# Kernel optimization log

Hardware: AMD Instinct MI355X
Metric: run time of the kernel (lower is better)

The kernel has to match this reference:

```python
import jax, jax.numpy as jnp
import numpy as np

N_NODES = 100000
N_EDGES = 1600000
D_IN = 128
D_OUT = 128


def setup_inputs() -> dict:
    key = jax.random.key(0)
    ks = jax.random.split(key, 8)
    x = jax.random.normal(ks[0], (N_NODES, D_IN), dtype=jnp.float32)
    edge_index = jax.random.randint(ks[1], (2, N_EDGES), 0, N_NODES, dtype=jnp.int64)
    s1 = 1.0 / np.sqrt(D_IN)
    s2 = 1.0 / np.sqrt(D_OUT)
    # SAGEConv: lin_l acts on aggregated neighbors (has bias), lin_r on self (no bias)
    Wl1 = jax.random.uniform(ks[2], (D_OUT, D_IN), jnp.float32, -s1, s1)
    Wr1 = jax.random.uniform(ks[3], (D_OUT, D_IN), jnp.float32, -s1, s1)
    b1 = jnp.zeros((D_OUT,), jnp.float32)
    Wl2 = jax.random.uniform(ks[4], (D_OUT, D_OUT), jnp.float32, -s2, s2)
    Wr2 = jax.random.uniform(ks[5], (D_OUT, D_OUT), jnp.float32, -s2, s2)
    b2 = jnp.zeros((D_OUT,), jnp.float32)
    return {"x": x, "edge_index": edge_index, "Wl1": Wl1, "Wr1": Wr1, "b1": b1,
            "Wl2": Wl2, "Wr2": Wr2, "b2": b2}


def _sage_conv(x, src, dst, Wl, Wr, b, n_nodes):
    # mean aggregation of source features at destination nodes
    agg = jax.ops.segment_sum(x[src], dst, num_segments=n_nodes)  # [N, d]
    deg = jax.ops.segment_sum(jnp.ones((src.shape[0],), x.dtype), dst, num_segments=n_nodes)
    mean = agg / jnp.maximum(deg, 1.0)[:, None]  # isolated nodes -> 0 (PyG scatter-mean)
    return mean @ Wl.T + b + x @ Wr.T


def reference(x, edge_index, Wl1, Wr1, b1, Wl2, Wr2, b2):
    src, dst = edge_index[0], edge_index[1]
    n = x.shape[0]
    h = _sage_conv(x, src, dst, Wl1, Wr1, b1, n)
    h = _sage_conv(h, src, dst, Wl2, Wr2, b2, n)
    return h
```

## Files before the change

kernel.cpp:

```cpp
#include <hip/hip_runtime.h>
#include <hip/hip_bf16.h>

#define D 128
#define SCAN_CHUNK 1024
#define TE 4096

typedef __attribute__((ext_vector_type(8))) short bf16x8;
typedef __attribute__((ext_vector_type(4))) float f32x4;
typedef __attribute__((ext_vector_type(2))) float f32x2;

__device__ __forceinline__ bool ei_is64(const int* ei32) {
    return (ei32[1] | ei32[3] | ei32[5] | ei32[7]) == 0;
}
__device__ __forceinline__ int get_idx(const void* ei, bool is64, long long pos) {
    return is64 ? (int)((const long long*)ei)[pos] : ((const int*)ei)[pos];
}

__global__ __launch_bounds__(256) void prep_kernel(
    const float* __restrict__ x, unsigned* __restrict__ xq, long long ND, int ncvt,
    const float* __restrict__ Wl1, const float* __restrict__ Wr1,
    const float* __restrict__ Wl2, const float* __restrict__ Wr2,
    ushort* __restrict__ Wf1, ushort* __restrict__ Wf2,
    const void* __restrict__ ei, int E, int NB, int NBLK, int SH,
    int* __restrict__ histT) {
    __shared__ int h[512];
    const int t = threadIdx.x;
    int bid = blockIdx.x;

    if (bid < ncvt) {
        long long i = ((long long)bid * 256 + t) * 8;
        if (i + 7 < ND) {
            float4 v0 = *reinterpret_cast<const float4*>(x + i);
            float4 v1 = *reinterpret_cast<const float4*>(x + i + 4);
            int p0 = __builtin_amdgcn_cvt_pk_fp8_f32(v0.x, v0.y, 0, false);
            p0 = __builtin_amdgcn_cvt_pk_fp8_f32(v0.z, v0.w, p0, true);
            int p1 = __builtin_amdgcn_cvt_pk_fp8_f32(v1.x, v1.y, 0, false);
            p1 = __builtin_amdgcn_cvt_pk_fp8_f32(v1.z, v1.w, p1, true);
            *reinterpret_cast<uint2*>(reinterpret_cast<unsigned char*>(xq) + i) =
                make_uint2((unsigned)p0, (unsigned)p1);
        } else {
            for (; i < ND; ++i) {
                int pk = __builtin_amdgcn_cvt_pk_fp8_f32(x[i], x[i], 0, false);
                reinterpret_cast<unsigned char*>(xq)[i] = (unsigned char)(pk & 0xff);
            }
        }
        return;
    }
    bid -= ncvt;
    if (bid < 32) {
        int gid = bid * 256 + t;
        int id = gid & 4095;
        const float* Wl = Wl1; const float* Wr = Wr1; ushort* Wf = Wf1;
        if (gid >= 4096) { Wl = Wl2; Wr = Wr2; Wf = Wf2; }
        int lane = id & 63, s = (id >> 6) & 7, j = id >> 9;
        int c = j * 16 + (lane & 15);
        int k = s * 32 + ((lane >> 4) << 3);
        const float* src = (k < 128) ? (Wl + c * 128 + k) : (Wr + c * 128 + (k - 128));
        float4 v0 = *reinterpret_cast<const float4*>(src);
        float4 v1 = *reinterpret_cast<const float4*>(src + 4);
        __hip_bfloat16 o[8];
        o[0] = __float2bfloat16(v0.x); o[1] = __float2bfloat16(v0.y);
        o[2] = __float2bfloat16(v0.z); o[3] = __float2bfloat16(v0.w);
        o[4] = __float2bfloat16(v1.x); o[5] = __float2bfloat16(v1.y);
        o[6] = __float2bfloat16(v1.z); o[7] = __float2bfloat16(v1.w);
        *reinterpret_cast<uint4*>(Wf + (size_t)id * 8) = *reinterpret_cast<uint4*>(o);
        return;
    }
    bid -= 32;
    for (int b = t; b < 512; b += 256) h[b] = 0;
    bool is64 = ei_is64((const int*)ei);
    __syncthreads();
    const int base = bid * TE;
    for (int i = t; i < TE; i += 256) {
        int e = base + i;
        if (e < E) {
            int d = get_idx(ei, is64, (long long)E + e);
            atomicAdd(&h[d >> SH], 1);
        }
    }
    __syncthreads();
    for (int b = t; b < NB; b += 256) histT[b * NBLK + bid] = h[b];
}

__global__ __launch_bounds__(256) void scan_partial_kernel(int* __restrict__ arr, int Ntot,
                                                           int* __restrict__ bsum) {
    __shared__ int ws[256];
    const int t = threadIdx.x;
    const int i0 = blockIdx.x * SCAN_CHUNK + t * 4;
    int4 v = {0, 0, 0, 0};
    if (i0 + 3 < Ntot) {
        v = *reinterpret_cast<const int4*>(arr + i0);
    } else {
        if (i0 < Ntot) v.x = arr[i0];
        if (i0 + 1 < Ntot) v.y = arr[i0 + 1];
        if (i0 + 2 < Ntot) v.z = arr[i0 + 2];
        if (i0 + 3 < Ntot) v.w = arr[i0 + 3];
    }
    ws[t] = v.x + v.y + v.z + v.w;
    __syncthreads();
    for (int off = 1; off < 256; off <<= 1) {
        int val = (t >= off) ? ws[t - off] : 0;
        __syncthreads();
        ws[t] += val;
        __syncthreads();
    }
    int ex = t ? ws[t - 1] : 0;
    int e0 = ex, e1 = ex + v.x, e2 = e1 + v.y, e3 = e2 + v.z;
    if (i0 + 3 < Ntot) {
        *reinterpret_cast<int4*>(arr + i0) = make_int4(e0, e1, e2, e3);
    } else {
        if (i0 < Ntot) arr[i0] = e0;
        if (i0 + 1 < Ntot) arr[i0 + 1] = e1;
        if (i0 + 2 < Ntot) arr[i0 + 2] = e2;
        if (i0 + 3 < Ntot) arr[i0 + 3] = e3;
    }
    if (t == 255) bsum[blockIdx.x] = ws[255];
}

__device__ __forceinline__ void scan_bsum_lds(const int* __restrict__ bsum, int nb2,
                                              int* sb) {
    const int t = threadIdx.x;
    sb[t] = (t < nb2) ? bsum[t] : 0;
    __syncthreads();
    for (int off = 1; off < 256; off <<= 1) {
        int v = (t >= off) ? sb[t - off] : 0;
        __syncthreads();
        sb[t] += v;
        __syncthreads();
    }
}

__global__ __launch_bounds__(256) void part_scatter_kernel(const void* __restrict__ ei, int E,
                                                           int NB, int NBLK, int SH,
                                                           const int* __restrict__ histT,
                                                           const int* __restrict__ bsum,
                                                           int nb2,
                                                           unsigned* __restrict__ ebuf) {
    __shared__ int cur[512];
    __shared__ int sb[256];
    const int t = threadIdx.x;
    bool is64 = ei_is64((const int*)ei);
    scan_bsum_lds(bsum, nb2, sb);
    for (int b = t; b < NB; b += 256) {
        int idx = b * NBLK + blockIdx.x;
        int c = idx >> 10;
        cur[b] = histT[idx] + (c ? sb[c - 1] : 0);
    }
    __syncthreads();
    const int base = blockIdx.x * TE;
    for (int i = t; i < TE; i += 256) {
        int e = base + i;
        if (e < E) {
            int s = get_idx(ei, is64, e);
            int d = get_idx(ei, is64, (long long)E + e);
            int pos = atomicAdd(&cur[d >> SH], 1);
            ebuf[pos] = (unsigned)s | ((unsigned)(d & ((1 << SH) - 1)) << 24);
        }
    }
}

__global__ __launch_bounds__(256) void bucket_csr_kernel(const unsigned* __restrict__ ebuf,
                                                         const int* __restrict__ histT,
                                                         const int* __restrict__ bsum,
                                                         int nb2,
                                                         int NB, int NBLK, int SH, int E,
                                                         int N, int* __restrict__ rs,
                                                         int* __restrict__ col) {
    const int b = blockIdx.x, t = threadIdx.x;
    const int nodes = 1 << SH;
    __shared__ int h[256];
    __shared__ int cur[256];
    __shared__ int sb[256];
    __shared__ int sse[2];
    scan_bsum_lds(bsum, nb2, sb);
    if (t == 0) {
        int i0 = b * NBLK;
        int c0 = i0 >> 10;
        sse[0] = histT[i0] + (c0 ? sb[c0 - 1] : 0);
        if (b + 1 < NB) {
            int i1 = (b + 1) * NBLK;
            int c1 = i1 >> 10;
            sse[1] = histT[i1] + (c1 ? sb[c1 - 1] : 0);
        } else {
            sse[1] = E;
        }
    }
    h[t] = 0;
    __syncthreads();
    const int bstart = sse[0], bend = sse[1];
    for (int i = bstart + t; i < bend; i += 256) {
        atomicAdd(&h[ebuf[i] >> 24], 1);
    }
    __syncthreads();
    for (int off = 1; off < nodes; off <<= 1) {
        int v = (t >= off) ? h[t - off] : 0;
        __syncthreads();
        h[t] += v;
        __syncthreads();
    }
    const int node0 = b << SH;
    {
        int node = node0 + t;
        if (node < N) rs[node] = bstart + h[t];
        cur[t] = bstart + (t ? h[t - 1] : 0);
    }
    __syncthreads();
    for (int i = bstart + t; i < bend; i += 256) {
        unsigned ed = ebuf[i];
        int pos = atomicAdd(&cur[ed >> 24], 1);
        col[pos] = (int)(ed & 0xFFFFFFu);
    }
}

__device__ __forceinline__ void acc8(f32x2& a0, f32x2& a1, f32x2& a2, f32x2& a3,
                                     uint2 d) {
    a0 += __builtin_amdgcn_cvt_pk_f32_fp8((int)d.x, false);
    a1 += __builtin_amdgcn_cvt_pk_f32_fp8((int)d.x, true);
    a2 += __builtin_amdgcn_cvt_pk_f32_fp8((int)d.y, false);
    a3 += __builtin_amdgcn_cvt_pk_f32_fp8((int)d.y, true);
}

__global__ __launch_bounds__(512) void aggregate_mean_fp8_kernel(
    const unsigned char* __restrict__ xq, const int* __restrict__ rs,
    const int* __restrict__ col, ushort* __restrict__ outm, int N) {
    __shared__ int s_start[32], s_end[32], s_map[32];
    const int t = threadIdx.x;
    if (t < 32) {
        int v = blockIdx.x * 32 + t;
        int st = 0, en = 0;
        if (v < N) { st = v ? rs[v - 1] : 0; en = rs[v]; }
        s_start[t] = st; s_end[t] = en;
    }
    __syncthreads();
    if (t < 32) {
        int d = s_end[t] - s_start[t];
        int r = 0;
#pragma unroll
        for (int j = 0; j < 32; ++j) {
            int dj = s_end[j] - s_start[j];
            r += (dj < d) || (dj == d && j < t);
        }
        s_map[r] = t;
    }
    __syncthreads();

    const int Q = t >> 4;
    const int li = s_map[Q];
    const int v = blockIdx.x * 32 + li;
    const int start = s_start[li], end = s_end[li];
    const unsigned lcoff = (unsigned)(t & 15) * 8u;

    f32x2 a0 = {0.f, 0.f}, a1 = {0.f, 0.f}, a2 = {0.f, 0.f}, a3 = {0.f, 0.f};
    int e = start;
    for (; e + 7 < end; e += 8) {
        int c0 = col[e], c1 = col[e + 1], c2 = col[e + 2], c3 = col[e + 3];
        int c4 = col[e + 4], c5 = col[e + 5], c6 = col[e + 6], c7 = col[e + 7];
        uint2 d0 = *reinterpret_cast<const uint2*>(xq + (((unsigned)c0) << 7) + lcoff);
        uint2 d1 = *reinterpret_cast<const uint2*>(xq + (((unsigned)c1) << 7) + lcoff);
        uint2 d2 = *reinterpret_cast<const uint2*>(xq + (((unsigned)c2) << 7) + lcoff);
        uint2 d3 = *reinterpret_cast<const uint2*>(xq + (((unsigned)c3) << 7) + lcoff);
        uint2 d4 = *reinterpret_cast<const uint2*>(xq + (((unsigned)c4) << 7) + lcoff);
        uint2 d5 = *reinterpret_cast<const uint2*>(xq + (((unsigned)c5) << 7) + lcoff);
        uint2 d6 = *reinterpret_cast<const uint2*>(xq + (((unsigned)c6) << 7) + lcoff);
        uint2 d7 = *reinterpret_cast<const uint2*>(xq + (((unsigned)c7) << 7) + lcoff);
        acc8(a0, a1, a2, a3, d0); acc8(a0, a1, a2, a3, d1);
        acc8(a0, a1, a2, a3, d2); acc8(a0, a1, a2, a3, d3);
        acc8(a0, a1, a2, a3, d4); acc8(a0, a1, a2, a3, d5);
        acc8(a0, a1, a2, a3, d6); acc8(a0, a1, a2, a3, d7);
    }
    if (e < end) {
        const int l = end - 1;
        int i1 = e + 1 < end ? e + 1 : l;
        int i2 = e + 2 < end ? e + 2 : l;
        int i3 = e + 3 < end ? e + 3 : l;
        int i4 = e + 4 < end ? e + 4 : l;
        int i5 = e + 5 < end ? e + 5 : l;
        int i6 = e + 6 < end ? e + 6 : l;
        int c0 = col[e], c1 = col[i1], c2 = col[i2], c3 = col[i3];
        int c4 = col[i4], c5 = col[i5], c6 = col[i6];
        uint2 d0 = *reinterpret_cast<const uint2*>(xq + (((unsigned)c0) << 7) + lcoff);
        uint2 d1 = *reinterpret_cast<const uint2*>(xq + (((unsigned)c1) << 7) + lcoff);
        uint2 d2 = *reinterpret_cast<const uint2*>(xq + (((unsigned)c2) << 7) + lcoff);
        uint2 d3 = *reinterpret_cast<const uint2*>(xq + (((unsigned)c3) << 7) + lcoff);
        uint2 d4 = *reinterpret_cast<const uint2*>(xq + (((unsigned)c4) << 7) + lcoff);
        uint2 d5 = *reinterpret_cast<const uint2*>(xq + (((unsigned)c5) << 7) + lcoff);
        uint2 d6 = *reinterpret_cast<const uint2*>(xq + (((unsigned)c6) << 7) + lcoff);
        d1.x = (e + 1 < end) ? d1.x : 0u; d1.y = (e + 1 < end) ? d1.y : 0u;
        d2.x = (e + 2 < end) ? d2.x : 0u; d2.y = (e + 2 < end) ? d2.y : 0u;
        d3.x = (e + 3 < end) ? d3.x : 0u; d3.y = (e + 3 < end) ? d3.y : 0u;
        d4.x = (e + 4 < end) ? d4.x : 0u; d4.y = (e + 4 < end) ? d4.y : 0u;
        d5.x = (e + 5 < end) ? d5.x : 0u; d5.y = (e + 5 < end) ? d5.y : 0u;
        d6.x = (e + 6 < end) ? d6.x : 0u; d6.y = (e + 6 < end) ? d6.y : 0u;
        acc8(a0, a1, a2, a3, d0); acc8(a0, a1, a2, a3, d1);
        acc8(a0, a1, a2, a3, d2); acc8(a0, a1, a2, a3, d3);
        acc8(a0, a1, a2, a3, d4); acc8(a0, a1, a2, a3, d5);
        acc8(a0, a1, a2, a3, d6);
    }
    if (v < N) {
        float inv = (end > start) ? 1.0f / (float)(end - start) : 0.f;
        __hip_bfloat16 o[8];
        o[0] = __float2bfloat16(a0.x * inv); o[1] = __float2bfloat16(a0.y * inv);
        o[2] = __float2bfloat16(a1.x * inv); o[3] = __float2bfloat16(a1.y * inv);
        o[4] = __float2bfloat16(a2.x * inv); o[5] = __float2bfloat16(a2.y * inv);
        o[6] = __float2bfloat16(a3.x * inv); o[7] = __float2bfloat16(a3.y * inv);
        *reinterpret_cast<uint4*>(outm + (size_t)v * D + ((t & 15) << 3)) =
            *reinterpret_cast<uint4*>(o);
    }
}

template <typename OutT, bool DUAL, bool SELFF32>
__global__ __launch_bounds__(512) void sage_mfma_kernel(
    const ushort* __restrict__ Ab, const void* __restrict__ Sb,
    const ushort* __restrict__ Wf, const float* __restrict__ bias,
    OutT* __restrict__ out, unsigned char* __restrict__ fq, int N) {
    __shared__ uint4 ldsB[4096];
    const int t = threadIdx.x;
    {
        const uint4* g = reinterpret_cast<const uint4*>(Wf);
#pragma unroll
        for (int i = 0; i < 8; ++i) ldsB[t + i * 512] = g[t + i * 512];
    }
    __syncthreads();

    const int lane = t & 63, w = t >> 6;
    const int lm = lane & 15;
    const int ksub = (lane >> 4) * 8;
    const int mbase = blockIdx.x * 128 + w * 16;

    int r0 = mbase + lm;
    if (r0 >= N) r0 = N - 1;

    f32x4 acc[8];
#pragma unroll
    for (int j = 0; j < 8; ++j) {
        float bv = bias[j * 16 + lm];
        acc[j] = {bv, bv, bv, bv};
    }

    const ushort* A0 = Ab + (size_t)r0 * D + ksub;
    const ushort* lB = reinterpret_cast<const ushort*>(ldsB) + lane * 8;

#pragma unroll
    for (int s = 0; s < 8; ++s) {
        bf16x8 a;
        if (s < 4) {
            a = *reinterpret_cast<const bf16x8*>(A0 + s * 32);
        } else if constexpr (SELFF32) {
            const float* S0 = (const float*)Sb + (size_t)r0 * D + (s - 4) * 32 + ksub;
            float4 v0 = *reinterpret_cast<const float4*>(S0);
            float4 v1 = *reinterpret_cast<const float4*>(S0 + 4);
            __hip_bfloat16 o[8];
            o[0] = __float2bfloat16(v0.x); o[1] = __float2bfloat16(v0.y);
            o[2] = __float2bfloat16(v0.z); o[3] = __float2bfloat16(v0.w);
            o[4] = __float2bfloat16(v1.x); o[5] = __float2bfloat16(v1.y);
            o[6] = __float2bfloat16(v1.z); o[7] = __float2bfloat16(v1.w);
            a = *reinterpret_cast<bf16x8*>(o);
        } else {
            const ushort* S0 = (const ushort*)Sb + (size_t)r0 * D + ksub;
            a = *reinterpret_cast<const bf16x8*>(S0 + (s - 4) * 32);
        }
#pragma unroll
        for (int j = 0; j < 8; ++j) {
            bf16x8 b = *reinterpret_cast<const bf16x8*>(lB + (j * 8 + s) * 512);
            acc[j] = __builtin_amdgcn_mfma_f32_16x16x32_bf16(a, b, acc[j], 0, 0, 0);
        }
    }

    const int rr = (lane >> 4) * 4;
#pragma unroll
    for (int r = 0; r < 4; ++r) {
        int row = mbase + rr + r;
        if (row < N) {
#pragma unroll
            for (int j = 0; j < 8; ++j) {
                float val = acc[j][r];
                if constexpr (sizeof(OutT) == 2)
                    out[(size_t)row * D + j * 16 + lm] = __float2bfloat16(val);
                else
                    out[(size_t)row * D + j * 16 + lm] = val;
                if constexpr (DUAL) {
                    int pk = __builtin_amdgcn_cvt_pk_fp8_f32(val, val, 0, false);
                    fq[(size_t)row * D + j * 16 + lm] = (unsigned char)(pk & 0xff);
                }
            }
        }
    }
}

extern "C" void kernel_launch(void* const* d_in, const int* in_sizes, int n_in,
                              void* d_out, int out_size, void* d_ws, size_t ws_size,
                              hipStream_t stream) {
    const float* x   = (const float*)d_in[0];
    const void*  ei  = d_in[1];
    const float* Wl1 = (const float*)d_in[2];
    const float* Wr1 = (const float*)d_in[3];
    const float* b1  = (const float*)d_in[4];
    const float* Wl2 = (const float*)d_in[5];
    const float* Wr2 = (const float*)d_in[6];
    const float* b2  = (const float*)d_in[7];
    float* out = (float*)d_out;

    const int N = in_sizes[0] / D;
    const int E = in_sizes[1] / 2;
    const long long ND = (long long)N * D;

    int SH = 8;
    while (((N + (1 << SH) - 1) >> SH) > 512) ++SH;
    const int NB = (N + (1 << SH) - 1) >> SH;
    const int NBLK = (E + TE - 1) / TE;
    const int Ntot = NB * NBLK;
    const int nb2 = (Ntot + SCAN_CHUNK - 1) / SCAN_CHUNK;

    ushort* meanb = (ushort*)d_ws;
    ushort* h1b   = meanb + ND;
    ushort* Wf1   = h1b + ND;
    ushort* Wf2   = Wf1 + 32768;
    int*    rs    = (int*)(Wf2 + 32768);
    int*    col   = rs + N;
    int*      histT = (int*)meanb;
    int*      bsum  = histT + Ntot;
    unsigned* ebuf  = (unsigned*)h1b;
    unsigned char* xq  = (unsigned char*)d_out;
    unsigned char* h1q = (unsigned char*)d_out + ND;

    const int ncvt = (int)((ND / 8 + 255) / 256);

    prep_kernel<<<ncvt + 32 + NBLK, 256, 0, stream>>>(
        x, (unsigned*)xq, ND, ncvt, Wl1, Wr1, Wl2, Wr2,
        Wf1, Wf2, ei, E, NB, NBLK, SH, histT);

    scan_partial_kernel<<<nb2, 256, 0, stream>>>(histT, Ntot, bsum);
    part_scatter_kernel<<<NBLK, 256, 0, stream>>>(ei, E, NB, NBLK, SH, histT, bsum, nb2, ebuf);
    bucket_csr_kernel<<<NB, 256, 0, stream>>>(ebuf, histT, bsum, nb2, NB, NBLK, SH, E, N, rs, col);

    const int agg_grid = (N + 31) / 32;
    const int gemm_grid = (N + 127) / 128;

    aggregate_mean_fp8_kernel<<<agg_grid, 512, 0, stream>>>(xq, rs, col, meanb, N);
    sage_mfma_kernel<__hip_bfloat16, true, true><<<gemm_grid, 512, 0, stream>>>(
        meanb, x, Wf1, b1, (__hip_bfloat16*)h1b, h1q, N);

    aggregate_mean_fp8_kernel<<<agg_grid, 512, 0, stream>>>(h1q, rs, col, meanb, N);
    sage_mfma_kernel<float, false, false><<<gemm_grid, 512, 0, stream>>>(
        meanb, h1b, Wf2, b2, out, nullptr, N);
}
```

Measured before the change: 164.0 us.

## Process two nodes per 16-lane group in aggregation, drop degree-sort scheduling

The mean-aggregation kernel now has each 16-thread group handle two destination nodes (v and v+16) with interleaved 8-edge gather batches, using 256-thread blocks instead of 512. The shared-memory degree ranking and its two __syncthreads are removed. The aim is more independent loads in flight per thread and less per-block setup. In exchange, per-thread register use goes up, and the two nodes in a group can have unbalanced degrees, which leaves lanes idle.

```diff
diff --git a/kernel.cpp b/kernel.cpp
--- a/kernel.cpp
+++ b/kernel.cpp
@@ -220,92 +220,107 @@
     a3 += __builtin_amdgcn_cvt_pk_f32_fp8((int)d.y, true);
 }
 
-__global__ __launch_bounds__(512) void aggregate_mean_fp8_kernel(
+__device__ __forceinline__ void gather_batch8(
+    const unsigned char* __restrict__ xq, const int* __restrict__ col, int e,
+    unsigned lcoff, f32x2& a0, f32x2& a1, f32x2& a2, f32x2& a3) {
+    int c0 = col[e], c1 = col[e + 1], c2 = col[e + 2], c3 = col[e + 3];
+    int c4 = col[e + 4], c5 = col[e + 5], c6 = col[e + 6], c7 = col[e + 7];
+    uint2 d0 = *reinterpret_cast<const uint2*>(xq + (((unsigned)c0) << 7) + lcoff);
+    uint2 d1 = *reinterpret_cast<const uint2*>(xq + (((unsigned)c1) << 7) + lcoff);
+    uint2 d2 = *reinterpret_cast<const uint2*>(xq + (((unsigned)c2) << 7) + lcoff);
+    uint2 d3 = *reinterpret_cast<const uint2*>(xq + (((unsigned)c3) << 7) + lcoff);
+    uint2 d4 = *reinterpret_cast<const uint2*>(xq + (((unsigned)c4) << 7) + lcoff);
+    uint2 d5 = *reinterpret_cast<const uint2*>(xq + (((unsigned)c5) << 7) + lcoff);
+    uint2 d6 = *reinterpret_cast<const uint2*>(xq + (((unsigned)c6) << 7) + lcoff);
+    uint2 d7 = *reinterpret_cast<const uint2*>(xq + (((unsigned)c7) << 7) + lcoff);
+    acc8(a0, a1, a2, a3, d0); acc8(a0, a1, a2, a3, d1);
+    acc8(a0, a1, a2, a3, d2); acc8(a0, a1, a2, a3, d3);
+    acc8(a0, a1, a2, a3, d4); acc8(a0, a1, a2, a3, d5);
+    acc8(a0, a1, a2, a3, d6); acc8(a0, a1, a2, a3, d7);
+}
+
+__device__ __forceinline__ void gather_masked(
+    const unsigned char* __restrict__ xq, const int* __restrict__ col, int e, int end,
+    unsigned lcoff, f32x2& a0, f32x2& a1, f32x2& a2, f32x2& a3) {
+    const int l = end - 1;
+    int i1 = e + 1 < end ? e + 1 : l;
+    int i2 = e + 2 < end ? e + 2 : l;
+    int i3 = e + 3 < end ? e + 3 : l;
+    int i4 = e + 4 < end ? e + 4 : l;
+    int i5 = e + 5 < end ? e + 5 : l;
+    int i6 = e + 6 < end ? e + 6 : l;
+    int c0 = col[e], c1 = col[i1], c2 = col[i2], c3 = col[i3];
+    int c4 = col[i4], c5 = col[i5], c6 = col[i6];
+    uint2 d0 = *reinterpret_cast<const uint2*>(xq + (((unsigned)c0) << 7) + lcoff);
+    uint2 d1 = *reinterpret_cast<const uint2*>(xq + (((unsigned)c1) << 7) + lcoff);
+    uint2 d2 = *reinterpret_cast<const uint2*>(xq + (((unsigned)c2) << 7) + lcoff);
+    uint2 d3 = *reinterpret_cast<const uint2*>(xq + (((unsigned)c3) << 7) + lcoff);
+    uint2 d4 = *reinterpret_cast<const uint2*>(xq + (((unsigned)c4) << 7) + lcoff);
+    uint2 d5 = *reinterpret_cast<const uint2*>(xq + (((unsigned)c5) << 7) + lcoff);
+    uint2 d6 = *reinterpret_cast<const uint2*>(xq + (((unsigned)c6) << 7) + lcoff);
+    d1.x = (e + 1 < end) ? d1.x : 0u; d1.y = (e + 1 < end) ? d1.y : 0u;
+    d2.x = (e + 2 < end) ? d2.x : 0u; d2.y = (e + 2 < end) ? d2.y : 0u;
+    d3.x = (e + 3 < end) ? d3.x : 0u; d3.y = (e + 3 < end) ? d3.y : 0u;
+    d4.x = (e + 4 < end) ? d4.x : 0u; d4.y = (e + 4 < end) ? d4.y : 0u;
+    d5.x = (e + 5 < end) ? d5.x : 0u; d5.y = (e + 5 < end) ? d5.y : 0u;
+    d6.x = (e + 6 < end) ? d6.x : 0u; d6.y = (e + 6 < end) ? d6.y : 0u;
+    acc8(a0, a1, a2, a3, d0); acc8(a0, a1, a2, a3, d1);
+    acc8(a0, a1, a2, a3, d2); acc8(a0, a1, a2, a3, d3);
+    acc8(a0, a1, a2, a3, d4); acc8(a0, a1, a2, a3, d5);
+    acc8(a0, a1, a2, a3, d6);
+}
+
+__device__ __forceinline__ void store_mean(ushort* __restrict__ outm, int v, int lc,
+                                           int deg, f32x2 a0, f32x2 a1, f32x2 a2,
+                                           f32x2 a3) {
+    float inv = (deg > 0) ? 1.0f / (float)deg : 0.f;
+    __hip_bfloat16 o[8];
+    o[0] = __float2bfloat16(a0.x * inv); o[1] = __float2bfloat16(a0.y * inv);
+    o[2] = __float2bfloat16(a1.x * inv); o[3] = __float2bfloat16(a1.y * inv);
+    o[4] = __float2bfloat16(a2.x * inv); o[5] = __float2bfloat16(a2.y * inv);
+    o[6] = __float2bfloat16(a3.x * inv); o[7] = __float2bfloat16(a3.y * inv);
+    *reinterpret_cast<uint4*>(outm + (size_t)v * D + (lc << 3)) =
+        *reinterpret_cast<uint4*>(o);
+}
+
+__global__ __launch_bounds__(256) void aggregate_mean_fp8_kernel(
     const unsigned char* __restrict__ xq, const int* __restrict__ rs,
     const int* __restrict__ col, ushort* __restrict__ outm, int N) {
-    __shared__ int s_start[32], s_end[32], s_map[32];
-    const int t = threadIdx.x;
-    if (t < 32) {
-        int v = blockIdx.x * 32 + t;
-        int st = 0, en = 0;
-        if (v < N) { st = v ? rs[v - 1] : 0; en = rs[v]; }
-        s_start[t] = st; s_end[t] = en;
-    }
-    __syncthreads();
-    if (t < 32) {
-        int d = s_end[t] - s_start[t];
-        int r = 0;
-#pragma unroll
-        for (int j = 0; j < 32; ++j) {
-            int dj = s_end[j] - s_start[j];
-            r += (dj < d) || (dj == d && j < t);
-        }
-        s_map[r] = t;
-    }
-    __syncthreads();
-
+    const int t = threadIdx.x;
     const int Q = t >> 4;
-    const int li = s_map[Q];
-    const int v = blockIdx.x * 32 + li;
-    const int start = s_start[li], end = s_end[li];
-    const unsigned lcoff = (unsigned)(t & 15) * 8u;
-
-    f32x2 a0 = {0.f, 0.f}, a1 = {0.f, 0.f}, a2 = {0.f, 0.f}, a3 = {0.f, 0.f};
-    int e = start;
-    for (; e + 7 < end; e += 8) {
-        int c0 = col[e], c1 = col[e + 1], c2 = col[e + 2], c3 = col[e + 3];
-        int c4 = col[e + 4], c5 = col[e + 5], c6 = col[e + 6], c7 = col[e + 7];
-        uint2 d0 = *reinterpret_cast<const uint2*>(xq + (((unsigned)c0) << 7) + lcoff);
-        uint2 d1 = *reinterpret_cast<const uint2*>(xq + (((unsigned)c1) << 7) + lcoff);
-        uint2 d2 = *reinterpret_cast<const uint2*>(xq + (((unsigned)c2) << 7) + lcoff);
-        uint2 d3 = *reinterpret_cast<const uint2*>(xq + (((unsigned)c3) << 7) + lcoff);
-        uint2 d4 = *reinterpret_cast<const uint2*>(xq + (((unsigned)c4) << 7) + lcoff);
-        uint2 d5 = *reinterpret_cast<const uint2*>(xq + (((unsigned)c5) << 7) + lcoff);
-        uint2 d6 = *reinterpret_cast<const uint2*>(xq + (((unsigned)c6) << 7) + lcoff);
-        uint2 d7 = *reinterpret_cast<const uint2*>(xq + (((unsigned)c7) << 7) + lcoff);
-        acc8(a0, a1, a2, a3, d0); acc8(a0, a1, a2, a3, d1);
-        acc8(a0, a1, a2, a3, d2); acc8(a0, a1, a2, a3, d3);
-        acc8(a0, a1, a2, a3, d4); acc8(a0, a1, a2, a3, d5);
-        acc8(a0, a1, a2, a3, d6); acc8(a0, a1, a2, a3, d7);
-    }
-    if (e < end) {
-        const int l = end - 1;
-        int i1 = e + 1 < end ? e + 1 : l;
-        int i2 = e + 2 < end ? e + 2 : l;
-        int i3 = e + 3 < end ? e + 3 : l;
-        int i4 = e + 4 < end ? e + 4 : l;
-        int i5 = e + 5 < end ? e + 5 : l;
-        int i6 = e + 6 < end ? e + 6 : l;
-        int c0 = col[e], c1 = col[i1], c2 = col[i2], c3 = col[i3];
-        int c4 = col[i4], c5 = col[i5], c6 = col[i6];
-        uint2 d0 = *reinterpret_cast<const uint2*>(xq + (((unsigned)c0) << 7) + lcoff);
-        uint2 d1 = *reinterpret_cast<const uint2*>(xq + (((unsigned)c1) << 7) + lcoff);
-        uint2 d2 = *reinterpret_cast<const uint2*>(xq + (((unsigned)c2) << 7) + lcoff);
-        uint2 d3 = *reinterpret_cast<const uint2*>(xq + (((unsigned)c3) << 7) + lcoff);
-        uint2 d4 = *reinterpret_cast<const uint2*>(xq + (((unsigned)c4) << 7) + lcoff);
-        uint2 d5 = *reinterpret_cast<const uint2*>(xq + (((unsigned)c5) << 7) + lcoff);
-        uint2 d6 = *reinterpret_cast<const uint2*>(xq + (((unsigned)c6) << 7) + lcoff);
-        d1.x = (e + 1 < end) ? d1.x : 0u; d1.y = (e + 1 < end) ? d1.y : 0u;
-        d2.x = (e + 2 < end) ? d2.x : 0u; d2.y = (e + 2 < end) ? d2.y : 0u;
-        d3.x = (e + 3 < end) ? d3.x : 0u; d3.y = (e + 3 < end) ? d3.y : 0u;
-        d4.x = (e + 4 < end) ? d4.x : 0u; d4.y = (e + 4 < end) ? d4.y : 0u;
-        d5.x = (e + 5 < end) ? d5.x : 0u; d5.y = (e + 5 < end) ? d5.y : 0u;
-        d6.x = (e + 6 < end) ? d6.x : 0u; d6.y = (e + 6 < end) ? d6.y : 0u;
-        acc8(a0, a1, a2, a3, d0); acc8(a0, a1, a2, a3, d1);
-        acc8(a0, a1, a2, a3, d2); acc8(a0, a1, a2, a3, d3);
-        acc8(a0, a1, a2, a3, d4); acc8(a0, a1, a2, a3, d5);
-        acc8(a0, a1, a2, a3, d6);
-    }
-    if (v < N) {
-        float inv = (end > start) ? 1.0f / (float)(end - start) : 0.f;
-        __hip_bfloat16 o[8];
-        o[0] = __float2bfloat16(a0.x * inv); o[1] = __float2bfloat16(a0.y * inv);
-        o[2] = __float2bfloat16(a1.x * inv); o[3] = __float2bfloat16(a1.y * inv);
-        o[4] = __float2bfloat16(a2.x * inv); o[5] = __float2bfloat16(a2.y * inv);
-        o[6] = __float2bfloat16(a3.x * inv); o[7] = __float2bfloat16(a3.y * inv);
-        *reinterpret_cast<uint4*>(outm + (size_t)v * D + ((t & 15) << 3)) =
-            *reinterpret_cast<uint4*>(o);
-    }
+    const int lc = t & 15;
+    const unsigned lcoff = (unsigned)lc * 8u;
+    const int vA = blockIdx.x * 32 + Q;
+    const int vB = vA + 16;
+
+    int sA = 0, nA = 0, sB = 0, nB = 0;
+    if (vA < N) { sA = vA ? rs[vA - 1] : 0; nA = rs[vA]; }
+    if (vB < N) { sB = rs[vB - 1]; nB = rs[vB]; }
+
+    f32x2 aA0 = {0.f, 0.f}, aA1 = {0.f, 0.f}, aA2 = {0.f, 0.f}, aA3 = {0.f, 0.f};
+    f32x2 aB0 = {0.f, 0.f}, aB1 = {0.f, 0.f}, aB2 = {0.f, 0.f}, aB3 = {0.f, 0.f};
+
+    int fA = (nA - sA) >> 3, fB = (nB - sB) >> 3;
+    int eA = sA, eB = sB;
+    const int common = fA < fB ? fA : fB;
+    for (int i = 0; i < common; ++i) {
+        gather_batch8(xq, col, eA, lcoff, aA0, aA1, aA2, aA3);
+        gather_batch8(xq, col, eB, lcoff, aB0, aB1, aB2, aB3);
+        eA += 8; eB += 8;
+    }
+    for (int i = common; i < fA; ++i) {
+        gather_batch8(xq, col, eA, lcoff, aA0, aA1, aA2, aA3);
+        eA += 8;
+    }
+    for (int i = common; i < fB; ++i) {
+        gather_batch8(xq, col, eB, lcoff, aB0, aB1, aB2, aB3);
+        eB += 8;
+    }
+    if (eA < nA) gather_masked(xq, col, eA, nA, lcoff, aA0, aA1, aA2, aA3);
+    if (eB < nB) gather_masked(xq, col, eB, nB, lcoff, aB0, aB1, aB2, aB3);
+
+    if (vA < N) store_mean(outm, vA, lc, nA - sA, aA0, aA1, aA2, aA3);
+    if (vB < N) store_mean(outm, vB, lc, nB - sB, aB0, aB1, aB2, aB3);
 }
 
 template <typename OutT, bool DUAL, bool SELFF32>
@@ -436,11 +451,11 @@
     const int agg_grid = (N + 31) / 32;
     const int gemm_grid = (N + 127) / 128;
 
-    aggregate_mean_fp8_kernel<<<agg_grid, 512, 0, stream>>>(xq, rs, col, meanb, N);
+    aggregate_mean_fp8_kernel<<<agg_grid, 256, 0, stream>>>(xq, rs, col, meanb, N);
     sage_mfma_kernel<__hip_bfloat16, true, true><<<gemm_grid, 512, 0, stream>>>(
         meanb, x, Wf1, b1, (__hip_bfloat16*)h1b, h1q, N);
 
-    aggregate_mean_fp8_kernel<<<agg_grid, 512, 0, stream>>>(h1q, rs, col, meanb, N);
+    aggregate_mean_fp8_kernel<<<agg_grid, 256, 0, stream>>>(h1q, rs, col, meanb, N);
     sage_mfma_kernel<float, false, false><<<gemm_grid, 512, 0, stream>>>(
         meanb, h1b, Wf2, b2, out, nullptr, N);
 }
```

Result: slower. 175.8 us (+7.2%).
